# Kernel optimization log

Hardware: AMD Instinct MI355X
Metric: run time of the kernel (lower is better)

## Reference

```python
import jax, jax.numpy as jnp
import numpy as np

N = 10000   # num_nodes (= input feature dim, identity-style features)
E = 320000  # edges (avg degree 32)
P = 200000  # candidate node pairs
H1, H2 = 32, 16


def gcn_conv(x, W, b, edge_index, num_nodes):
    # PyG GCNConv: add self-loops, symmetric D^-1/2 (A+I) D^-1/2 normalization,
    # linear transform, scatter-add aggregation, then bias.
    loop = jnp.arange(num_nodes)
    src = jnp.concatenate([edge_index[0], loop])
    dst = jnp.concatenate([edge_index[1], loop])
    deg = jax.ops.segment_sum(jnp.ones_like(src, dtype=x.dtype), dst,
                              num_segments=num_nodes)  # includes self-loop, so deg >= 1
    dinv = jax.lax.rsqrt(deg)
    norm = dinv[src] * dinv[dst]                       # [E+N]
    h = x @ W                                          # [N, out]
    out = jax.ops.segment_sum(h[src] * norm[:, None], dst, num_segments=num_nodes)
    return out + b


def setup_inputs() -> dict:
    key = jax.random.key(0)
    ks = jax.random.split(key, 9)
    x = jax.random.normal(ks[0], (N, N), dtype=jnp.float32)
    edge_index = jax.random.randint(ks[1], (2, E), 0, N)
    pair_index = jax.random.randint(ks[2], (P, 2), 0, N)
    W1 = jax.random.normal(ks[3], (N, H1), dtype=jnp.float32) * 0.01
    b1 = jnp.zeros((H1,), jnp.float32)
    W2 = jax.random.normal(ks[4], (H1, H2), dtype=jnp.float32) * 0.1
    b2 = jnp.zeros((H2,), jnp.float32)
    Wfc = jax.random.normal(ks[5], (2 * H2, 1), dtype=jnp.float32) * 0.1
    bfc = jnp.zeros((1,), jnp.float32)
    return {"x": x, "edge_index": edge_index, "pair_index": pair_index,
            "W1": W1, "b1": b1, "W2": W2, "b2": b2, "Wfc": Wfc, "bfc": bfc}


def reference(x, edge_index, pair_index, W1, b1, W2, b2, Wfc, bfc):
    h = jax.nn.relu(gcn_conv(x, W1, b1, edge_index, N))   # [N, 32]
    h = gcn_conv(h, W2, b2, edge_index, N)                # [N, 16]
    pair = jnp.concatenate([h[pair_index[:, 0]], h[pair_index[:, 1]]], axis=1)  # [P, 32]
    return jax.nn.sigmoid(pair @ Wfc + bfc)               # [P, 1]
```

## Files before the change

### kernel.cpp

```cpp
#include <hip/hip_runtime.h>
#include <math.h>

#define NN 10000
#define EE 320000
#define PP 200000
#define NTILES 320

typedef __attribute__((ext_vector_type(8))) short bf8v;
typedef __attribute__((ext_vector_type(4))) float f4v;

#define GLOAD_LDS16(gsrc, ldst)                                                        \
    __builtin_amdgcn_global_load_lds((const __attribute__((address_space(1))) void*)(gsrc), \
                                     (__attribute__((address_space(3))) void*)(ldst), 16, 0, 0)

__device__ __forceinline__ ushort f2bf(float f) {
    uint u = __float_as_uint(f);
    return (ushort)((u + 0x7fffu + ((u >> 16) & 1u)) >> 16);
}

__global__ void k_deg_count(const int* __restrict__ dst, int* __restrict__ degi) {
    int e = blockIdx.x * blockDim.x + threadIdx.x;
    if (e < EE) atomicAdd(&degi[dst[e]], 1);
}

__global__ void k_dinv(const int* __restrict__ degi, float* __restrict__ dinv) {
    int n = blockIdx.x * blockDim.x + threadIdx.x;
    if (n < NN) dinv[n] = rsqrtf((float)(degi[n] + 1));
}

__global__ void k_wprep(const float* __restrict__ W1, ushort* __restrict__ wf) {
    int t = blockIdx.x * blockDim.x + threadIdx.x;
    if (t >= NTILES * 2 * 64 * 8) return;
    int e = t & 7, lane = (t >> 3) & 63, ct = (t >> 9) & 1, g = t >> 10;
    int col = ct * 16 + (lane & 15);
    int k = g * 32 + (lane >> 4) * 8 + e;
    wf[t] = (k < NN) ? f2bf(W1[(long)k * 32 + col]) : (ushort)0;
}

__global__ __launch_bounds__(256) void k_gemm1(const float* __restrict__ x,
                                               const ushort* __restrict__ wf,
                                               const float* __restrict__ zp,
                                               float* __restrict__ h1_pre) {
    __shared__ __align__(16) float  xs[4][2][32][32];
    __shared__ __align__(16) ushort ws[4][2][1024];
    const int tid = threadIdx.x;
    const int lane = tid & 63;
    const int w = tid >> 6;
    const int lr = lane >> 3;
    const int s = lane & 7;
    const int fl = lane & 15;
    const int khi = lane >> 4;
    const int row0 = blockIdx.x * 128 + w * 32;
    const int k_begin = blockIdx.y * 640;
    const int k_end = min(NN, k_begin + 640);
    const int g0 = blockIdx.y * 20;
    const int nt = (k_end - k_begin + 31) >> 5;
    const long NN2 = (long)NN * NN;

    f4v acc[2][2];
#pragma unroll
    for (int a = 0; a < 2; ++a)
#pragma unroll
        for (int b = 0; b < 2; ++b) acc[a][b] = (f4v){0.f, 0.f, 0.f, 0.f};

    auto stage = [&](int buf, int t) {
        const int k0 = k_begin + t * 32;
#pragma unroll
        for (int j = 0; j < 4; ++j) {
            int rl = j * 8 + lr;
            int c4 = s ^ (rl & 7);
            long flat = (long)(row0 + rl) * NN + k0 + c4 * 4;
            const float* src = (flat + 4 <= NN2) ? (x + flat) : zp;
            GLOAD_LDS16(src, &xs[w][buf][j * 8][0]);
        }
        const int g = g0 + t;
#pragma unroll
        for (int ct = 0; ct < 2; ++ct)
            GLOAD_LDS16(wf + ((long)(g * 2 + ct) * 64 + lane) * 8, &ws[w][buf][ct * 512]);
    };
    auto compute = [&](int buf) {
        bf8v b0 = *(const bf8v*)&ws[w][buf][lane * 8];
        bf8v b1 = *(const bf8v*)&ws[w][buf][512 + lane * 8];
#pragma unroll
        for (int rt = 0; rt < 2; ++rt) {
            const int rowl = rt * 16 + fl;
            const float4* xr = (const float4*)&xs[w][buf][rowl][0];
            float4 f0 = xr[(khi * 2)     ^ (rowl & 7)];
            float4 f1 = xr[(khi * 2 + 1) ^ (rowl & 7)];
            union { bf8v v; ushort u[8]; } a;
            a.u[0] = f2bf(f0.x); a.u[1] = f2bf(f0.y); a.u[2] = f2bf(f0.z); a.u[3] = f2bf(f0.w);
            a.u[4] = f2bf(f1.x); a.u[5] = f2bf(f1.y); a.u[6] = f2bf(f1.z); a.u[7] = f2bf(f1.w);
            acc[rt][0] = __builtin_amdgcn_mfma_f32_16x16x32_bf16(a.v, b0, acc[rt][0], 0, 0, 0);
            acc[rt][1] = __builtin_amdgcn_mfma_f32_16x16x32_bf16(a.v, b1, acc[rt][1], 0, 0, 0);
        }
    };

    stage(0, 0);
    int buf = 0;
    for (int t = 0; t < nt; ++t) {
        if (t + 1 < nt) {
            stage(buf ^ 1, t + 1);
            asm volatile("s_waitcnt vmcnt(6)" ::: "memory");
        } else {
            asm volatile("s_waitcnt vmcnt(0)" ::: "memory");
        }
        __builtin_amdgcn_sched_barrier(0);
        compute(buf);
        buf ^= 1;
    }

#pragma unroll
    for (int rt = 0; rt < 2; ++rt) {
        const int gbase = row0 + rt * 16 + khi * 4;
#pragma unroll
        for (int ct = 0; ct < 2; ++ct) {
            const int col = ct * 16 + fl;
#pragma unroll
            for (int r = 0; r < 4; ++r) {
                const int g = gbase + r;
                if (g < NN) atomicAdd(&h1_pre[g * 32 + col], acc[rt][ct][r]);
            }
        }
    }
}

__global__ void k_selfinit1(const float* __restrict__ h1_pre, const float* __restrict__ dinv,
                            float* __restrict__ out1) {
    int t = blockIdx.x * blockDim.x + threadIdx.x;
    if (t < NN * 32) {
        int n = t >> 5;
        float di = dinv[n];
        out1[t] = di * di * h1_pre[t];
    }
}

__global__ void k_scatter1(const int* __restrict__ src, const int* __restrict__ dst,
                           const float* __restrict__ dinv, const float* __restrict__ h1_pre,
                           float* __restrict__ out1) {
    int t = blockIdx.x * blockDim.x + threadIdx.x;
    if (t >= EE * 32) return;
    int e = t >> 5, c = t & 31;
    int s = src[e], d = dst[e];
    float nrm = dinv[s] * dinv[d];
    atomicAdd(&out1[d * 32 + c], h1_pre[s * 32 + c] * nrm);
}

__global__ void k_bias_relu1(float* __restrict__ out1, const float* __restrict__ b1) {
    int t = blockIdx.x * blockDim.x + threadIdx.x;
    if (t < NN * 32) out1[t] = fmaxf(out1[t] + b1[t & 31], 0.f);
}

__global__ __launch_bounds__(256) void k_gemm2(const float* __restrict__ out1,
                                               const float* __restrict__ W2,
                                               float* __restrict__ h2_pre) {
    __shared__ float w2s[512];
    int tid = threadIdx.x;
    w2s[tid] = W2[tid & 511];
    if (tid < 256) w2s[256 + tid] = W2[256 + tid];
    __syncthreads();
    int c = tid & 15, yloc = tid >> 4;
    int n = blockIdx.x * 16 + yloc;
    if (n < NN) {
        float a = 0.f;
#pragma unroll
        for (int k = 0; k < 32; ++k) a += out1[n * 32 + k] * w2s[k * 16 + c];
        h2_pre[n * 16 + c] = a;
    }
}

__global__ void k_selfinit2(const float* __restrict__ h2_pre, const float* __restrict__ dinv,
                            float* __restrict__ out2) {
    int t = blockIdx.x * blockDim.x + threadIdx.x;
    if (t < NN * 16) {
        int n = t >> 4;
        float di = dinv[n];
        out2[t] = di * di * h2_pre[t];
    }
}

__global__ void k_scatter2(const int* __restrict__ src, const int* __restrict__ dst,
                           const float* __restrict__ dinv, const float* __restrict__ h2_pre,
                           float* __restrict__ out2) {
    int t = blockIdx.x * blockDim.x + threadIdx.x;
    if (t >= EE * 16) return;
    int e = t >> 4, c = t & 15;
    int s = src[e], d = dst[e];
    float nrm = dinv[s] * dinv[d];
    atomicAdd(&out2[d * 16 + c], h2_pre[s * 16 + c] * nrm);
}

__global__ void k_final2(const float* __restrict__ out2, const float* __restrict__ b2,
                         const float* __restrict__ Wfc, float* __restrict__ s_arr,
                         float* __restrict__ t_arr) {
    int n = blockIdx.x * blockDim.x + threadIdx.x;
    if (n >= NN) return;
    float s = 0.f, t = 0.f;
#pragma unroll
    for (int c = 0; c < 16; ++c) {
        float v = out2[n * 16 + c] + b2[c];
        s += v * Wfc[c];
        t += v * Wfc[16 + c];
    }
    s_arr[n] = s;
    t_arr[n] = t;
}

__global__ void k_pairs(const int* __restrict__ pair, const float* __restrict__ s_arr,
                        const float* __restrict__ t_arr, const float* __restrict__ bfc,
                        float* __restrict__ out) {
    int p = blockIdx.x * blockDim.x + threadIdx.x;
    if (p >= PP) return;
    const int2 ab = ((const int2*)pair)[p];
    float z = s_arr[ab.x] + t_arr[ab.y] + bfc[0];
    out[p] = 1.f / (1.f + expf(-z));
}

extern "C" void kernel_launch(void* const* d_in, const int* in_sizes, int n_in,
                              void* d_out, int out_size, void* d_ws, size_t ws_size,
                              hipStream_t stream) {
    const float* x    = (const float*)d_in[0];
    const int*   edge = (const int*)d_in[1];
    const int*   pair = (const int*)d_in[2];
    const float* W1   = (const float*)d_in[3];
    const float* b1   = (const float*)d_in[4];
    const float* W2   = (const float*)d_in[5];
    const float* b2   = (const float*)d_in[6];
    const float* Wfc  = (const float*)d_in[7];
    const float* bfc  = (const float*)d_in[8];
    float* out = (float*)d_out;
    float* ws  = (float*)d_ws;

    const int* src = edge;
    const int* dst = edge + EE;

    int*    degi   = (int*)ws;
    float*  dinv   = ws + NN;
    float*  h1_pre = ws + 2 * NN;
    float*  out1   = ws + 34 * NN;
    float*  h2_pre = ws + 66 * NN;
    float*  out2   = ws + 82 * NN;
    float*  s_arr  = ws + 98 * NN;
    float*  t_arr  = ws + 99 * NN;
    float*  zp     = ws + 100 * NN;
    ushort* w1f    = (ushort*)(ws + 100 * NN + 256);

    hipMemsetAsync(degi, 0, NN * sizeof(int), stream);
    hipMemsetAsync(h1_pre, 0, NN * 32 * sizeof(float), stream);
    hipMemsetAsync(zp, 0, 1024, stream);

    k_deg_count<<<(EE + 255) / 256, 256, 0, stream>>>(dst, degi);
    k_dinv<<<(NN + 255) / 256, 256, 0, stream>>>(degi, dinv);
    k_wprep<<<(NTILES * 2 * 64 * 8 + 255) / 256, 256, 0, stream>>>(W1, w1f);

    k_gemm1<<<dim3(79, 16), 256, 0, stream>>>(x, w1f, zp, h1_pre);

    k_selfinit1<<<(NN * 32 + 255) / 256, 256, 0, stream>>>(h1_pre, dinv, out1);
    k_scatter1<<<(EE * 32 + 255) / 256, 256, 0, stream>>>(src, dst, dinv, h1_pre, out1);
    k_bias_relu1<<<(NN * 32 + 255) / 256, 256, 0, stream>>>(out1, b1);

    k_gemm2<<<(NN + 15) / 16, 256, 0, stream>>>(out1, W2, h2_pre);

    k_selfinit2<<<(NN * 16 + 255) / 256, 256, 0, stream>>>(h2_pre, dinv, out2);
    k_scatter2<<<(EE * 16 + 255) / 256, 256, 0, stream>>>(src, dst, dinv, h2_pre, out2);

    k_final2<<<(NN + 255) / 256, 256, 0, stream>>>(out2, b2, Wfc, s_arr, t_arr);
    k_pairs<<<(PP + 255) / 256, 256, 0, stream>>>(pair, s_arr, t_arr, bfc, out);
}
```

Measured before the change: 198.9 us.

## Restructure first GEMM: fp16 MFMA, triple-buffered 128-wide K tiles, split-K partials

The x@W1 GEMM is rebuilt. Each block now preloads its whole W1 slice into LDS once. Each wave handles 16 rows with K tiles of 128, using a three-buffer global-to-LDS pipeline with explicit waitcnt scheduling. Inputs are converted to fp16 instead of bf16, and the MFMA changes to the f16 variant. Atomic accumulation into h1_pre is replaced by per-split partial stores that the self-init kernel sums. This drops the memset and atomic contention but adds extra partial-buffer traffic, and fp16 can overflow for large values.

```diff
diff --git a/kernel.cpp b/kernel.cpp
--- a/kernel.cpp
+++ b/kernel.cpp
@@ -6,16 +6,17 @@
 #define PP 200000
 #define NTILES 320
 
-typedef __attribute__((ext_vector_type(8))) short bf8v;
+typedef _Float16 h8v __attribute__((ext_vector_type(8)));
 typedef __attribute__((ext_vector_type(4))) float f4v;
 
 #define GLOAD_LDS16(gsrc, ldst)                                                        \
     __builtin_amdgcn_global_load_lds((const __attribute__((address_space(1))) void*)(gsrc), \
                                      (__attribute__((address_space(3))) void*)(ldst), 16, 0, 0)
 
-__device__ __forceinline__ ushort f2bf(float f) {
-    uint u = __float_as_uint(f);
-    return (ushort)((u + 0x7fffu + ((u >> 16) & 1u)) >> 16);
+__device__ __forceinline__ ushort f2h(float f) {
+    union { _Float16 h; ushort u; } c;
+    c.h = (_Float16)f;
+    return c.u;
 }
 
 __global__ void k_deg_count(const int* __restrict__ dst, int* __restrict__ degi) {
@@ -34,103 +35,105 @@
     int e = t & 7, lane = (t >> 3) & 63, ct = (t >> 9) & 1, g = t >> 10;
     int col = ct * 16 + (lane & 15);
     int k = g * 32 + (lane >> 4) * 8 + e;
-    wf[t] = (k < NN) ? f2bf(W1[(long)k * 32 + col]) : (ushort)0;
+    wf[t] = (k < NN) ? f2h(W1[(long)k * 32 + col]) : (ushort)0;
 }
 
 __global__ __launch_bounds__(256) void k_gemm1(const float* __restrict__ x,
-                                               const ushort* __restrict__ wf,
+                                               const ushort* __restrict__ w1f,
                                                const float* __restrict__ zp,
-                                               float* __restrict__ h1_pre) {
-    __shared__ __align__(16) float  xs[4][2][32][32];
-    __shared__ __align__(16) ushort ws[4][2][1024];
+                                               float* __restrict__ h1_part) {
+    __shared__ __align__(16) float  xs[4 * 3 * 2080];
+    __shared__ __align__(16) ushort wlds[2560 * 8];
     const int tid = threadIdx.x;
     const int lane = tid & 63;
     const int w = tid >> 6;
-    const int lr = lane >> 3;
-    const int s = lane & 7;
     const int fl = lane & 15;
     const int khi = lane >> 4;
-    const int row0 = blockIdx.x * 128 + w * 32;
-    const int k_begin = blockIdx.y * 640;
-    const int k_end = min(NN, k_begin + 640);
-    const int g0 = blockIdx.y * 20;
-    const int nt = (k_end - k_begin + 31) >> 5;
+    const int ks = blockIdx.y;
+    const int wrow0 = blockIdx.x * 64 + w * 16;
+    const int k_begin = ks * 640;
     const long NN2 = (long)NN * NN;
 
-    f4v acc[2][2];
-#pragma unroll
-    for (int a = 0; a < 2; ++a)
-#pragma unroll
-        for (int b = 0; b < 2; ++b) acc[a][b] = (f4v){0.f, 0.f, 0.f, 0.f};
-
+    f4v acc0 = (f4v){0.f, 0.f, 0.f, 0.f};
+    f4v acc1 = (f4v){0.f, 0.f, 0.f, 0.f};
+
+#pragma unroll
+    for (int i = 0; i < 10; ++i) {
+        const int ul = i * 256 + w * 64 + lane;
+        const ushort* srcw =
+            w1f + (((long)(ks * 20 + (ul >> 7)) * 2 + ((ul >> 6) & 1)) * 64 + lane) * 8;
+        GLOAD_LDS16(srcw, &wlds[(long)(i * 256 + w * 64) * 8]);
+    }
+    __syncthreads();
+
+    const int sub = lane >> 5;
+    const int kof = (lane & 31) * 4;
     auto stage = [&](int buf, int t) {
-        const int k0 = k_begin + t * 32;
-#pragma unroll
-        for (int j = 0; j < 4; ++j) {
-            int rl = j * 8 + lr;
-            int c4 = s ^ (rl & 7);
-            long flat = (long)(row0 + rl) * NN + k0 + c4 * 4;
+        const int k0 = k_begin + t * 128;
+        float* dst = &xs[(w * 3 + buf) * 2080];
+#pragma unroll
+        for (int p = 0; p < 8; ++p) {
+            long flat = (long)(wrow0 + p * 2 + sub) * NN + k0 + kof;
             const float* src = (flat + 4 <= NN2) ? (x + flat) : zp;
-            GLOAD_LDS16(src, &xs[w][buf][j * 8][0]);
-        }
-        const int g = g0 + t;
-#pragma unroll
-        for (int ct = 0; ct < 2; ++ct)
-            GLOAD_LDS16(wf + ((long)(g * 2 + ct) * 64 + lane) * 8, &ws[w][buf][ct * 512]);
-    };
-    auto compute = [&](int buf) {
-        bf8v b0 = *(const bf8v*)&ws[w][buf][lane * 8];
-        bf8v b1 = *(const bf8v*)&ws[w][buf][512 + lane * 8];
-#pragma unroll
-        for (int rt = 0; rt < 2; ++rt) {
-            const int rowl = rt * 16 + fl;
-            const float4* xr = (const float4*)&xs[w][buf][rowl][0];
-            float4 f0 = xr[(khi * 2)     ^ (rowl & 7)];
-            float4 f1 = xr[(khi * 2 + 1) ^ (rowl & 7)];
-            union { bf8v v; ushort u[8]; } a;
-            a.u[0] = f2bf(f0.x); a.u[1] = f2bf(f0.y); a.u[2] = f2bf(f0.z); a.u[3] = f2bf(f0.w);
-            a.u[4] = f2bf(f1.x); a.u[5] = f2bf(f1.y); a.u[6] = f2bf(f1.z); a.u[7] = f2bf(f1.w);
-            acc[rt][0] = __builtin_amdgcn_mfma_f32_16x16x32_bf16(a.v, b0, acc[rt][0], 0, 0, 0);
-            acc[rt][1] = __builtin_amdgcn_mfma_f32_16x16x32_bf16(a.v, b1, acc[rt][1], 0, 0, 0);
+            GLOAD_LDS16(src, dst + p * 260);
         }
     };
-
-    stage(0, 0);
-    int buf = 0;
-    for (int t = 0; t < nt; ++t) {
-        if (t + 1 < nt) {
-            stage(buf ^ 1, t + 1);
-            asm volatile("s_waitcnt vmcnt(6)" ::: "memory");
-        } else {
-            asm volatile("s_waitcnt vmcnt(0)" ::: "memory");
+    auto compute = [&](int buf, int t) {
+        const float4* xrow =
+            (const float4*)&xs[(w * 3 + buf) * 2080 + (fl >> 1) * 260 + (fl & 1) * 128];
+#pragma unroll
+        for (int kk = 0; kk < 4; ++kk) {
+            const int gl = t * 4 + kk;
+            h8v b0 = *(const h8v*)&wlds[((gl * 2 + 0) * 64 + lane) * 8];
+            h8v b1 = *(const h8v*)&wlds[((gl * 2 + 1) * 64 + lane) * 8];
+            float4 f0 = xrow[kk * 8 + khi * 2];
+            float4 f1 = xrow[kk * 8 + khi * 2 + 1];
+            union { h8v v; _Float16 h[8]; } a;
+            a.h[0] = (_Float16)f0.x; a.h[1] = (_Float16)f0.y;
+            a.h[2] = (_Float16)f0.z; a.h[3] = (_Float16)f0.w;
+            a.h[4] = (_Float16)f1.x; a.h[5] = (_Float16)f1.y;
+            a.h[6] = (_Float16)f1.z; a.h[7] = (_Float16)f1.w;
+            acc0 = __builtin_amdgcn_mfma_f32_16x16x32_f16(a.v, b0, acc0, 0, 0, 0);
+            acc1 = __builtin_amdgcn_mfma_f32_16x16x32_f16(a.v, b1, acc1, 0, 0, 0);
         }
-        __builtin_amdgcn_sched_barrier(0);
-        compute(buf);
-        buf ^= 1;
-    }
-
-#pragma unroll
-    for (int rt = 0; rt < 2; ++rt) {
-        const int gbase = row0 + rt * 16 + khi * 4;
-#pragma unroll
-        for (int ct = 0; ct < 2; ++ct) {
-            const int col = ct * 16 + fl;
-#pragma unroll
-            for (int r = 0; r < 4; ++r) {
-                const int g = gbase + r;
-                if (g < NN) atomicAdd(&h1_pre[g * 32 + col], acc[rt][ct][r]);
-            }
+    };
+
+#define WAITV(n) asm volatile("s_waitcnt vmcnt(" #n ")" ::: "memory"); __builtin_amdgcn_sched_barrier(0)
+#define WAITL()  asm volatile("s_waitcnt lgkmcnt(0)" ::: "memory");    __builtin_amdgcn_sched_barrier(0)
+
+    stage(0, 0); stage(1, 1); stage(2, 2);
+    WAITV(16); compute(0, 0); WAITL(); stage(0, 3);
+    WAITV(16); compute(1, 1); WAITL(); stage(1, 4);
+    WAITV(16); compute(2, 2);
+    WAITV(8);  compute(0, 3);
+    WAITV(0);  compute(1, 4);
+#undef WAITV
+#undef WAITL
+
+    const long pbase = (long)ks * NN * 32;
+#pragma unroll
+    for (int ct = 0; ct < 2; ++ct) {
+        f4v a = ct ? acc1 : acc0;
+        const int col = ct * 16 + fl;
+#pragma unroll
+        for (int r = 0; r < 4; ++r) {
+            int g = wrow0 + khi * 4 + r;
+            if (g < NN) h1_part[pbase + (long)g * 32 + col] = a[r];
         }
     }
 }
 
-__global__ void k_selfinit1(const float* __restrict__ h1_pre, const float* __restrict__ dinv,
-                            float* __restrict__ out1) {
+__global__ void k_selfinit1(const float* __restrict__ h1_part, const float* __restrict__ dinv,
+                            float* __restrict__ h1_pre, float* __restrict__ out1) {
     int t = blockIdx.x * blockDim.x + threadIdx.x;
     if (t < NN * 32) {
+        float sum = 0.f;
+#pragma unroll
+        for (int ks = 0; ks < 16; ++ks) sum += h1_part[(long)ks * NN * 32 + t];
         int n = t >> 5;
         float di = dinv[n];
-        out1[t] = di * di * h1_pre[t];
+        h1_pre[t] = sum;
+        out1[t] = di * di * sum;
     }
 }
 
@@ -233,28 +236,28 @@
     const int* src = edge;
     const int* dst = edge + EE;
 
-    int*    degi   = (int*)ws;
-    float*  dinv   = ws + NN;
-    float*  h1_pre = ws + 2 * NN;
-    float*  out1   = ws + 34 * NN;
-    float*  h2_pre = ws + 66 * NN;
-    float*  out2   = ws + 82 * NN;
-    float*  s_arr  = ws + 98 * NN;
-    float*  t_arr  = ws + 99 * NN;
-    float*  zp     = ws + 100 * NN;
-    ushort* w1f    = (ushort*)(ws + 100 * NN + 256);
+    int*    degi    = (int*)ws;
+    float*  dinv    = ws + NN;
+    float*  h1_pre  = ws + 2 * NN;
+    float*  out1    = ws + 34 * NN;
+    float*  h2_pre  = ws + 66 * NN;
+    float*  out2    = ws + 82 * NN;
+    float*  s_arr   = ws + 98 * NN;
+    float*  t_arr   = ws + 99 * NN;
+    float*  zp      = ws + 100 * NN;
+    ushort* w1f     = (ushort*)(ws + 100 * NN + 256);
+    float*  h1_part = ws + 100 * NN + 256 + 163840;
 
     hipMemsetAsync(degi, 0, NN * sizeof(int), stream);
-    hipMemsetAsync(h1_pre, 0, NN * 32 * sizeof(float), stream);
     hipMemsetAsync(zp, 0, 1024, stream);
 
     k_deg_count<<<(EE + 255) / 256, 256, 0, stream>>>(dst, degi);
     k_dinv<<<(NN + 255) / 256, 256, 0, stream>>>(degi, dinv);
     k_wprep<<<(NTILES * 2 * 64 * 8 + 255) / 256, 256, 0, stream>>>(W1, w1f);
 
-    k_gemm1<<<dim3(79, 16), 256, 0, stream>>>(x, w1f, zp, h1_pre);
-
-    k_selfinit1<<<(NN * 32 + 255) / 256, 256, 0, stream>>>(h1_pre, dinv, out1);
+    k_gemm1<<<dim3(157, 16), 256, 0, stream>>>(x, w1f, zp, h1_part);
+
+    k_selfinit1<<<(NN * 32 + 255) / 256, 256, 0, stream>>>(h1_part, dinv, h1_pre, out1);
     k_scatter1<<<(EE * 32 + 255) / 256, 256, 0, stream>>>(src, dst, dinv, h1_pre, out1);
     k_bias_relu1<<<(NN * 32 + 255) / 256, 256, 0, stream>>>(out1, b1);
 
```

New measurement: 208.7 us. 4.9% more time.
